# Optimization experiments

Hardware: AMD Instinct MI355X
Metric: run time of the kernel (lower is better)

The kernel has to match this reference:

```python
import jax, jax.numpy as jnp
import numpy as np

N, E, D, H = 100000, 1600000, 128, 2  # nodes, edges, channels (in=out), heads
NEG_SLOPE = 0.2
EPS = 1e-16


def setup_inputs() -> dict:
    key = jax.random.key(0)
    ks = jax.random.split(key, 12)
    s = 1.0 / np.sqrt(D)
    return {
        "x": jax.random.normal(ks[0], (N, D), jnp.float32),
        "edge_index": jax.random.randint(ks[1], (2, E), 0, N, jnp.int64),
        "gamma": jnp.ones((D,), jnp.float32),
        "beta": jnp.zeros((D,), jnp.float32),
        "Wl": jax.random.normal(ks[2], (D, H * D), jnp.float32) * s,
        "bl": jnp.zeros((H * D,), jnp.float32),
        "Wr": jax.random.normal(ks[3], (D, H * D), jnp.float32) * s,
        "br": jnp.zeros((H * D,), jnp.float32),
        "att": jax.random.normal(ks[4], (H, D), jnp.float32) * s,
        "res_W": jax.random.normal(ks[5], (D, D), jnp.float32) * s,
        "bias": jnp.zeros((D,), jnp.float32),
    }


def _segment_softmax(alpha, seg, num_segments):
    m = jax.ops.segment_max(alpha, seg, num_segments=num_segments)
    a = jnp.exp(alpha - m[seg])
    z = jax.ops.segment_sum(a, seg, num_segments=num_segments)
    return a / (z[seg] + EPS)


def reference(x, edge_index, gamma, beta, Wl, bl, Wr, br, att, res_W, bias):
    n = x.shape[0]
    residual = x
    # per-node LayerNorm -> ReLU
    mu = x.mean(-1, keepdims=True)
    var = ((x - mu) ** 2).mean(-1, keepdims=True)
    h = (x - mu) * jax.lax.rsqrt(var + 1e-5) * gamma + beta
    h = jax.nn.relu(h)
    # GATv2: per-node linear transforms [N,H,D]
    xl = (h @ Wl + bl).reshape(n, H, D)  # source-side
    xr = (h @ Wr + br).reshape(n, H, D)  # target-side
    src, dst = edge_index[0], edge_index[1]
    e = jax.nn.leaky_relu(xl[src] + xr[dst], NEG_SLOPE)  # [E,H,D]
    alpha = jnp.einsum('ehd,hd->eh', e, att)             # [E,H]
    alpha = _segment_softmax(alpha, dst, n)
    msg = xl[src] * alpha[..., None]                     # [E,H,D]
    out = jax.ops.segment_sum(msg, dst, num_segments=n)  # [N,H,D]
    out = out.mean(axis=1)                               # concat=False -> mean heads
    out = out + h @ res_W + bias                         # GATv2 internal residual + bias
    return residual + out
```

## Files before the change

### kernel.cpp

```cpp
#include <hip/hip_runtime.h>
#include <hip/hip_bf16.h>
#include <cstdint>
#include <cstddef>

#define DCH 128
#define NHEADS 2
#define NEG_SLOPE 0.2f

typedef __attribute__((ext_vector_type(8))) short short8v;
typedef __attribute__((ext_vector_type(4))) float f32x4;
typedef _Float16 h2 __attribute__((ext_vector_type(2)));
typedef _Float16 h4 __attribute__((ext_vector_type(4)));

__device__ __forceinline__ unsigned short f2bf(float f) {
    union { float f; unsigned int i; } v; v.f = f;
    unsigned int r = v.i + 0x7fffu + ((v.i >> 16) & 1u);
    return (unsigned short)(r >> 16);
}
__device__ __forceinline__ unsigned short f2h_bits(float f) {
    _Float16 h = (_Float16)f;
    union { _Float16 h; unsigned short u; } v; v.h = h; return v.u;
}

__device__ __forceinline__ h2 lrelu2(h2 v, h2 ns) {
    h2 f = v * ns;
#if __has_builtin(__builtin_elementwise_max)
    return __builtin_elementwise_max(v, f);
#else
    h2 r; r[0] = v[0] > f[0] ? v[0] : f[0]; r[1] = v[1] > f[1] ? v[1] : f[1];
    return r;
#endif
}
__device__ __forceinline__ float dot4h(h2 a0, h2 a1, h2 b0, h2 b1) {
#if __has_builtin(__builtin_amdgcn_fdot2)
    return __builtin_amdgcn_fdot2(a0, b0, __builtin_amdgcn_fdot2(a1, b1, 0.f, false), false);
#else
    return (float)a0[0]*(float)b0[0] + (float)a0[1]*(float)b0[1]
         + (float)a1[0]*(float)b1[0] + (float)a1[1]*(float)b1[1];
#endif
}

__device__ __forceinline__ float halfsum(float p) {
    p += __int_as_float(__builtin_amdgcn_update_dpp(
            0, __float_as_int(p), 0x121, 0xF, 0xF, false));
    p += __int_as_float(__builtin_amdgcn_update_dpp(
            0, __float_as_int(p), 0x122, 0xF, 0xF, false));
    p += __int_as_float(__builtin_amdgcn_update_dpp(
            0, __float_as_int(p), 0x124, 0xF, 0xF, false));
    p += __int_as_float(__builtin_amdgcn_update_dpp(
            0, __float_as_int(p), 0x128, 0xF, 0xF, false));
    p += __int_as_float(__builtin_amdgcn_ds_swizzle(
            __float_as_int(p), 0x401F));
    return p;
}

__global__ void prep_and_zero(const float* __restrict__ Wl, const float* __restrict__ Wr,
                              const float* __restrict__ resW,
                              unsigned short* __restrict__ wfrag,
                              int* __restrict__ cnt, int n) {
    if (blockIdx.x >= 40) {
        int i = (blockIdx.x - 40) * 256 + threadIdx.x;
        if (i < n) cnt[i] = 0;
        return;
    }
    int gid  = blockIdx.x * 256 + threadIdx.x;
    int lane = gid & 63;
    int f    = gid >> 6;
    int ks   = f & 3;
    int ct   = f >> 2;
    int col  = ct * 16 + (lane & 15);
    int k0   = ks * 32 + (lane >> 4) * 8;
    const float* W; int ldB, c;
    if (col < 256)      { W = Wl;   ldB = 256; c = col; }
    else if (col < 512) { W = Wr;   ldB = 256; c = col - 256; }
    else                { W = resW; ldB = 128; c = col - 512; }
    unsigned short tmp[8];
#pragma unroll
    for (int j = 0; j < 8; ++j) tmp[j] = f2bf(W[(size_t)(k0 + j) * ldB + c]);
    ushort4* dst = (ushort4*)(wfrag + (size_t)gid * 8);
    dst[0] = make_ushort4(tmp[0], tmp[1], tmp[2], tmp[3]);
    dst[1] = make_ushort4(tmp[4], tmp[5], tmp[6], tmp[7]);
}

__launch_bounds__(256)
__global__ void gemm_fill(const float* __restrict__ x,
                          const float* __restrict__ gamma, const float* __restrict__ beta,
                          const unsigned short* __restrict__ wfrag,
                          const float* __restrict__ bl, const float* __restrict__ br,
                          const float* __restrict__ bias,
                          unsigned short* __restrict__ xl, unsigned short* __restrict__ xr,
                          float* __restrict__ out, int n,
                          const int* __restrict__ srcIdx, const int* __restrict__ dstIdx,
                          int* __restrict__ fillc, int* __restrict__ sbuf, int E, int nrb) {
    __shared__ __align__(16) unsigned short As[128 * 128];

    if ((int)blockIdx.x >= nrb) {
        int i = (blockIdx.x - nrb) * 256 + threadIdx.x;
        int E4 = E >> 2;
        if (i < E4) {
            int4 d = ((const int4*)dstIdx)[i];
            int4 s = ((const int4*)srcIdx)[i];
            sbuf[atomicAdd(&fillc[d.x], 1)] = s.x;
            sbuf[atomicAdd(&fillc[d.y], 1)] = s.y;
            sbuf[atomicAdd(&fillc[d.z], 1)] = s.z;
            sbuf[atomicAdd(&fillc[d.w], 1)] = s.w;
        }
        if (i < (E & 3)) {
            int e = E4 * 4 + i;
            sbuf[atomicAdd(&fillc[dstIdx[e]], 1)] = srcIdx[e];
        }
        return;
    }

    int row0 = blockIdx.x * 128;
    int tid  = threadIdx.x;

    {
        int r  = tid >> 5;
        int k4 = (tid & 31) * 4;
        float4 g4  = *(const float4*)(gamma + k4);
        float4 be4 = *(const float4*)(beta + k4);
#pragma unroll
        for (int i = 0; i < 16; ++i) {
            int row  = r + i * 8;
            int grow = row0 + row;
            float4 a = (grow < n) ? *(const float4*)(x + (size_t)grow * DCH + k4)
                                  : make_float4(0.f, 0.f, 0.f, 0.f);
            float s  = a.x + a.y + a.z + a.w;
            float sq = a.x * a.x + a.y * a.y + a.z * a.z + a.w * a.w;
#pragma unroll
            for (int msk = 16; msk; msk >>= 1) {
                s  += __shfl_xor(s, msk);
                sq += __shfl_xor(sq, msk);
            }
            float mu = s * (1.f / DCH);
            float rs = rsqrtf(sq * (1.f / DCH) - mu * mu + 1e-5f);
            ushort4 u;
            u.x = f2bf(fmaxf((a.x - mu) * rs * g4.x + be4.x, 0.f));
            u.y = f2bf(fmaxf((a.y - mu) * rs * g4.y + be4.y, 0.f));
            u.z = f2bf(fmaxf((a.z - mu) * rs * g4.z + be4.z, 0.f));
            u.w = f2bf(fmaxf((a.w - mu) * rs * g4.w + be4.w, 0.f));
            int byteoff = row * 256 + ((k4 * 2) ^ ((row & 7) << 4));
            *(ushort4*)((char*)As + byteoff) = u;
        }
    }
    __syncthreads();

    int wv = tid >> 6, lane = tid & 63;

    short8v afrag[2][4];
#pragma unroll
    for (int g = 0; g < 2; ++g) {
        int arow = wv * 32 + g * 16 + (lane & 15);
#pragma unroll
        for (int ks = 0; ks < 4; ++ks) {
            int kbyte = (ks * 64 + (lane >> 4) * 16) ^ ((arow & 7) << 4);
            afrag[g][ks] = *(const short8v*)((const char*)As + arow * 256 + kbyte);
        }
    }

    int node0 = row0 + wv * 32 + (lane & 15);
    int node1 = node0 + 16;
    bool v0 = node0 < n, v1 = node1 < n;
    int cq = (lane >> 4) << 2;

#pragma unroll 2
    for (int ct = 0; ct < 40; ++ct) {
        const unsigned short* bp = wfrag + ((size_t)(ct * 4) * 64 + lane) * 8;
        short8v b0 = *(const short8v*)(bp);
        short8v b1 = *(const short8v*)(bp + 64 * 8);
        short8v b2 = *(const short8v*)(bp + 128 * 8);
        short8v b3 = *(const short8v*)(bp + 192 * 8);
        f32x4 acc0 = {0.f, 0.f, 0.f, 0.f};
        f32x4 acc1 = {0.f, 0.f, 0.f, 0.f};
        acc0 = __builtin_amdgcn_mfma_f32_16x16x32_bf16(b0, afrag[0][0], acc0, 0, 0, 0);
        acc1 = __builtin_amdgcn_mfma_f32_16x16x32_bf16(b0, afrag[1][0], acc1, 0, 0, 0);
        acc0 = __builtin_amdgcn_mfma_f32_16x16x32_bf16(b1, afrag[0][1], acc0, 0, 0, 0);
        acc1 = __builtin_amdgcn_mfma_f32_16x16x32_bf16(b1, afrag[1][1], acc1, 0, 0, 0);
        acc0 = __builtin_amdgcn_mfma_f32_16x16x32_bf16(b2, afrag[0][2], acc0, 0, 0, 0);
        acc1 = __builtin_amdgcn_mfma_f32_16x16x32_bf16(b2, afrag[1][2], acc1, 0, 0, 0);
        acc0 = __builtin_amdgcn_mfma_f32_16x16x32_bf16(b3, afrag[0][3], acc0, 0, 0, 0);
        acc1 = __builtin_amdgcn_mfma_f32_16x16x32_bf16(b3, afrag[1][3], acc1, 0, 0, 0);

        int c0 = ct * 16 + cq;
        if (ct < 32) {
            unsigned short* dst; int c; const float* bv;
            if (ct < 16) { dst = xl; c = c0;       bv = bl; }
            else         { dst = xr; c = c0 - 256; bv = br; }
            float4 bb = *(const float4*)(bv + c);
            if (v0) {
                ushort4 u = make_ushort4(f2h_bits(acc0[0] + bb.x), f2h_bits(acc0[1] + bb.y),
                                         f2h_bits(acc0[2] + bb.z), f2h_bits(acc0[3] + bb.w));
                *(ushort4*)(dst + (size_t)node0 * 256 + c) = u;
            }
            if (v1) {
                ushort4 u = make_ushort4(f2h_bits(acc1[0] + bb.x), f2h_bits(acc1[1] + bb.y),
                                         f2h_bits(acc1[2] + bb.z), f2h_bits(acc1[3] + bb.w));
                *(ushort4*)(dst + (size_t)node1 * 256 + c) = u;
            }
        } else {
            int c = c0 - 512;
            float4 bb = *(const float4*)(bias + c);
            if (v0) {
                float4 xv = *(const float4*)(x + (size_t)node0 * DCH + c);
                float4 o = make_float4(acc0[0] + bb.x + xv.x, acc0[1] + bb.y + xv.y,
                                       acc0[2] + bb.z + xv.z, acc0[3] + bb.w + xv.w);
                *(float4*)(out + (size_t)node0 * DCH + c) = o;
            }
            if (v1) {
                float4 xv = *(const float4*)(x + (size_t)node1 * DCH + c);
                float4 o = make_float4(acc1[0] + bb.x + xv.x, acc1[1] + bb.y + xv.y,
                                       acc1[2] + bb.z + xv.z, acc1[3] + bb.w + xv.w);
                *(float4*)(out + (size_t)node1 * DCH + c) = o;
            }
        }
    }
}

__global__ void hist_dst(const int* __restrict__ dst, int* __restrict__ cnt, int E) {
    int i = blockIdx.x * blockDim.x + threadIdx.x;
    int E4 = E >> 2;
    if (i < E4) {
        int4 d = ((const int4*)dst)[i];
        atomicAdd(&cnt[d.x], 1); atomicAdd(&cnt[d.y], 1);
        atomicAdd(&cnt[d.z], 1); atomicAdd(&cnt[d.w], 1);
    }
    if (i < (E & 3)) atomicAdd(&cnt[dst[E4 * 4 + i]], 1);
}

__global__ void scan_block(const int* __restrict__ cnt, int* __restrict__ offs,
                           int* __restrict__ bsum, int n) {
    __shared__ int sm[256];
    int t = threadIdx.x;
    int i = blockIdx.x * 256 + t;
    int v = (i < n) ? cnt[i] : 0;
    sm[t] = v;
    __syncthreads();
#pragma unroll
    for (int d = 1; d < 256; d <<= 1) {
        int add = (t >= d) ? sm[t - d] : 0;
        __syncthreads();
        sm[t] += add;
        __syncthreads();
    }
    if (i < n) offs[i] = sm[t] - v;
    if (t == 255) bsum[blockIdx.x] = sm[t];
}

__global__ void scan_bsum_par(int* __restrict__ bsum, int nb) {
    __shared__ int sm[512];
    int t = threadIdx.x;
    if (nb <= 512) {
        int v = (t < nb) ? bsum[t] : 0;
        sm[t] = v;
        __syncthreads();
#pragma unroll
        for (int d = 1; d < 512; d <<= 1) {
            int add = (t >= d) ? sm[t - d] : 0;
            __syncthreads();
            sm[t] += add;
            __syncthreads();
        }
        if (t < nb) bsum[t] = sm[t] - v;
    } else if (t == 0) {
        int acc = 0;
        for (int i = 0; i < nb; ++i) { int v = bsum[i]; bsum[i] = acc; acc += v; }
    }
}

__global__ void scan_add(int* __restrict__ offs, int* __restrict__ fillc,
                         const int* __restrict__ bsum, int n, int E) {
    int i = blockIdx.x * 256 + threadIdx.x;
    if (i < n) {
        int v = offs[i] + bsum[blockIdx.x];
        offs[i]  = v;
        fillc[i] = v;
    }
    if (i == 0) offs[n] = E;
}

__launch_bounds__(256)
__global__ void gat_aggregate(const int* __restrict__ offs, const int* __restrict__ sbuf,
                              const unsigned short* __restrict__ xl_,
                              const unsigned short* __restrict__ xr_,
                              const float* __restrict__ att,
                              float* __restrict__ out, int n) {
    const _Float16* xl = (const _Float16*)xl_;
    const _Float16* xr = (const _Float16*)xr_;
    int lane = threadIdx.x & 63;
    int wid  = __builtin_amdgcn_readfirstlane((blockIdx.x * blockDim.x + threadIdx.x) >> 6);
    int nw   = (gridDim.x * blockDim.x) >> 6;

    const float LOG2E = 1.4426950408889634f;
    float4 af = *(const float4*)(att + lane * 4);
    h2 av0 = {(_Float16)(af.x * LOG2E), (_Float16)(af.y * LOG2E)};
    h2 av1 = {(_Float16)(af.z * LOG2E), (_Float16)(af.w * LOG2E)};
    h2 ns  = {(_Float16)NEG_SLOPE, (_Float16)NEG_SLOPE};

    for (int t = wid; t < n; t += nw) {
        int beg = offs[t];
        int end = offs[t + 1];
        if (beg == end) continue;
        h4 r4 = *(const h4*)(xr + (size_t)t * 256 + lane * 4);
        h2 r0 = __builtin_shufflevector(r4, r4, 0, 1);
        h2 r1 = __builtin_shufflevector(r4, r4, 2, 3);

        float m = -INFINITY, z = 0.f;
        float4 acc = make_float4(0.f, 0.f, 0.f, 0.f);

        auto process4 = [&](h4 l0, h4 l1, h4 l2, h4 l3) {
            float p0 = dot4h(lrelu2(__builtin_shufflevector(l0, l0, 0, 1) + r0, ns),
                             lrelu2(__builtin_shufflevector(l0, l0, 2, 3) + r1, ns), av0, av1);
            float p1 = dot4h(lrelu2(__builtin_shufflevector(l1, l1, 0, 1) + r0, ns),
                             lrelu2(__builtin_shufflevector(l1, l1, 2, 3) + r1, ns), av0, av1);
            float p2 = dot4h(lrelu2(__builtin_shufflevector(l2, l2, 0, 1) + r0, ns),
                             lrelu2(__builtin_shufflevector(l2, l2, 2, 3) + r1, ns), av0, av1);
            float p3 = dot4h(lrelu2(__builtin_shufflevector(l3, l3, 0, 1) + r0, ns),
                             lrelu2(__builtin_shufflevector(l3, l3, 2, 3) + r1, ns), av0, av1);
            p0 = halfsum(p0); p1 = halfsum(p1); p2 = halfsum(p2); p3 = halfsum(p3);
            float pm = fmaxf(fmaxf(p0, p1), fmaxf(p2, p3));
            if (__any(pm - m > 11.5f)) {
                float mn = fmaxf(m, pm);
                float sc = __builtin_amdgcn_exp2f(m - mn);
                z *= sc;
                acc.x *= sc; acc.y *= sc; acc.z *= sc; acc.w *= sc;
                m = mn;
            }
            float w0 = __builtin_amdgcn_exp2f(p0 - m);
            float w1 = __builtin_amdgcn_exp2f(p1 - m);
            float w2 = __builtin_amdgcn_exp2f(p2 - m);
            float w3 = __builtin_amdgcn_exp2f(p3 - m);
            z += (w0 + w1) + (w2 + w3);
            acc.x = fmaf((float)l0[0], w0, acc.x); acc.y = fmaf((float)l0[1], w0, acc.y);
            acc.z = fmaf((float)l0[2], w0, acc.z); acc.w = fmaf((float)l0[3], w0, acc.w);
            acc.x = fmaf((float)l1[0], w1, acc.x); acc.y = fmaf((float)l1[1], w1, acc.y);
            acc.z = fmaf((float)l1[2], w1, acc.z); acc.w = fmaf((float)l1[3], w1, acc.w);
            acc.x = fmaf((float)l2[0], w2, acc.x); acc.y = fmaf((float)l2[1], w2, acc.y);
            acc.z = fmaf((float)l2[2], w2, acc.z); acc.w = fmaf((float)l2[3], w2, acc.w);
            acc.x = fmaf((float)l3[0], w3, acc.x); acc.y = fmaf((float)l3[1], w3, acc.y);
            acc.z = fmaf((float)l3[2], w3, acc.z); acc.w = fmaf((float)l3[3], w3, acc.w);
        };

        int j = beg;
        h4 c0, c1, c2, c3;
        bool have = (j + 4 <= end);
        if (have) {
            int s0 = sbuf[j], s1 = sbuf[j + 1], s2 = sbuf[j + 2], s3 = sbuf[j + 3];
            c0 = *(const h4*)(xl + (size_t)s0 * 256 + lane * 4);
            c1 = *(const h4*)(xl + (size_t)s1 * 256 + lane * 4);
            c2 = *(const h4*)(xl + (size_t)s2 * 256 + lane * 4);
            c3 = *(const h4*)(xl + (size_t)s3 * 256 + lane * 4);
        }
        for (; j + 8 <= end; j += 4) {
            int s0 = sbuf[j + 4], s1 = sbuf[j + 5], s2 = sbuf[j + 6], s3 = sbuf[j + 7];
            h4 n0 = *(const h4*)(xl + (size_t)s0 * 256 + lane * 4);
            h4 n1 = *(const h4*)(xl + (size_t)s1 * 256 + lane * 4);
            h4 n2 = *(const h4*)(xl + (size_t)s2 * 256 + lane * 4);
            h4 n3 = *(const h4*)(xl + (size_t)s3 * 256 + lane * 4);
            process4(c0, c1, c2, c3);
            c0 = n0; c1 = n1; c2 = n2; c3 = n3;
        }
        if (have) { process4(c0, c1, c2, c3); j += 4; }
        for (; j < end; ++j) {
            int s = sbuf[j];
            h4 l0 = *(const h4*)(xl + (size_t)s * 256 + lane * 4);
            float p = dot4h(lrelu2(__builtin_shufflevector(l0, l0, 0, 1) + r0, ns),
                            lrelu2(__builtin_shufflevector(l0, l0, 2, 3) + r1, ns), av0, av1);
            p = halfsum(p);
            if (__any(p - m > 11.5f)) {
                float mn = fmaxf(m, p);
                float sc = __builtin_amdgcn_exp2f(m - mn);
                z *= sc;
                acc.x *= sc; acc.y *= sc; acc.z *= sc; acc.w *= sc;
                m = mn;
            }
            float w = __builtin_amdgcn_exp2f(p - m);
            z += w;
            acc.x = fmaf((float)l0[0], w, acc.x); acc.y = fmaf((float)l0[1], w, acc.y);
            acc.z = fmaf((float)l0[2], w, acc.z); acc.w = fmaf((float)l0[3], w, acc.w);
        }
        float inv = 0.5f / (z + 1e-16f);
        acc.x *= inv; acc.y *= inv; acc.z *= inv; acc.w *= inv;
        acc.x += __shfl_xor(acc.x, 32);
        acc.y += __shfl_xor(acc.y, 32);
        acc.z += __shfl_xor(acc.z, 32);
        acc.w += __shfl_xor(acc.w, 32);
        if (lane < 32) {
            float4* o = (float4*)(out + (size_t)t * DCH + lane * 4);
            float4 cur = *o;
            cur.x += acc.x; cur.y += acc.y; cur.z += acc.z; cur.w += acc.w;
            *o = cur;
        }
    }
}

extern "C" void kernel_launch(void* const* d_in, const int* in_sizes, int n_in,
                              void* d_out, int out_size, void* d_ws, size_t ws_size,
                              hipStream_t stream) {
    const float* x     = (const float*)d_in[0];
    const int*   ei    = (const int*)d_in[1];
    const float* gamma = (const float*)d_in[2];
    const float* beta  = (const float*)d_in[3];
    const float* Wl    = (const float*)d_in[4];
    const float* bl    = (const float*)d_in[5];
    const float* Wr    = (const float*)d_in[6];
    const float* br    = (const float*)d_in[7];
    const float* att   = (const float*)d_in[8];
    const float* resW  = (const float*)d_in[9];
    const float* bias  = (const float*)d_in[10];
    float* out = (float*)d_out;

    int n = in_sizes[0] / DCH;
    int E = in_sizes[1] / 2;
    const int* src = ei;
    const int* dstIdx = ei + E;

    char* ws = (char*)d_ws;
    size_t off = 0;
    auto alloc = [&](size_t bytes) -> void* {
        void* p = ws + off;
        off = (off + bytes + 255) & ~(size_t)255;
        return p;
    };

    int nb = (n + 255) / 256;

    unsigned short* xl = (unsigned short*)alloc((size_t)n * 256 * 2);
    unsigned short* xr = (unsigned short*)alloc((size_t)n * 256 * 2);
    unsigned short* wfrag = (unsigned short*)alloc(160 * 64 * 8 * 2);
    int* cnt   = (int*)alloc((size_t)n * 4);
    int* offs  = (int*)alloc((size_t)(n + 1) * 4);
    int* bsum  = (int*)alloc((size_t)nb * 4);
    int* fillc = (int*)alloc((size_t)n * 4);
    int* sbuf  = (int*)alloc((size_t)E * 4);

    prep_and_zero<<<40 + nb, 256, 0, stream>>>(Wl, Wr, resW, wfrag, cnt, n);
    int ethr = (E / 4 + 255) / 256 + 1;
    hist_dst<<<ethr, 256, 0, stream>>>(dstIdx, cnt, E);
    scan_block<<<nb, 256, 0, stream>>>(cnt, offs, bsum, n);
    scan_bsum_par<<<1, 512, 0, stream>>>(bsum, nb);
    scan_add<<<nb, 256, 0, stream>>>(offs, fillc, bsum, n, E);

    int nrb = (n + 127) / 128;
    gemm_fill<<<nrb + ethr, 256, 0, stream>>>(x, gamma, beta, wfrag, bl, br, bias,
                                              xl, xr, out, n,
                                              src, dstIdx, fillc, sbuf, E, nrb);
    gat_aggregate<<<2048, 256, 0, stream>>>(offs, sbuf, xl, xr, att, out, n);
}
```

Baseline: 349.9 us.

## Stage GEMM epilogue through swizzled LDS for coalesced 16-byte global stores

The GEMM epilogue now writes the MFMA results (xl/xr in fp16, and the residual output in fp32) into a swizzled shared-memory tile first. The block then copies the tile out row-contiguously with 16-byte vector stores, and adds x to the residual output during that copy. Before, each lane wrote scattered 8- or 16-byte fragments per column tile, which produced poorly coalesced global writes. The cost is extra LDS traffic and several block-wide barriers per column group, which can serialize MFMA work against the stores.

Measured after the change: 324.8 us. 7.2% less time.

```diff
diff --git a/kernel.cpp b/kernel.cpp
--- a/kernel.cpp
+++ b/kernel.cpp
@@ -92,7 +92,7 @@
                           float* __restrict__ out, int n,
                           const int* __restrict__ srcIdx, const int* __restrict__ dstIdx,
                           int* __restrict__ fillc, int* __restrict__ sbuf, int E, int nrb) {
-    __shared__ __align__(16) unsigned short As[128 * 128];
+    __shared__ __align__(16) unsigned char smem[128 * 256];
 
     if ((int)blockIdx.x >= nrb) {
         int i = (blockIdx.x - nrb) * 256 + threadIdx.x;
@@ -114,6 +114,7 @@
 
     int row0 = blockIdx.x * 128;
     int tid  = threadIdx.x;
+    unsigned short* As = (unsigned short*)smem;
 
     {
         int r  = tid >> 5;
@@ -158,62 +159,95 @@
             afrag[g][ks] = *(const short8v*)((const char*)As + arow * 256 + kbyte);
         }
     }
-
-    int node0 = row0 + wv * 32 + (lane & 15);
-    int node1 = node0 + 16;
-    bool v0 = node0 < n, v1 = node1 < n;
+    __syncthreads();
+
+    int nodeL0 = wv * 32 + (lane & 15);
+    int nodeL1 = nodeL0 + 16;
     int cq = (lane >> 4) << 2;
 
-#pragma unroll 2
-    for (int ct = 0; ct < 40; ++ct) {
+    auto mfma_ct = [&](int ct, f32x4& a0, f32x4& a1) {
         const unsigned short* bp = wfrag + ((size_t)(ct * 4) * 64 + lane) * 8;
         short8v b0 = *(const short8v*)(bp);
         short8v b1 = *(const short8v*)(bp + 64 * 8);
         short8v b2 = *(const short8v*)(bp + 128 * 8);
         short8v b3 = *(const short8v*)(bp + 192 * 8);
-        f32x4 acc0 = {0.f, 0.f, 0.f, 0.f};
-        f32x4 acc1 = {0.f, 0.f, 0.f, 0.f};
-        acc0 = __builtin_amdgcn_mfma_f32_16x16x32_bf16(b0, afrag[0][0], acc0, 0, 0, 0);
-        acc1 = __builtin_amdgcn_mfma_f32_16x16x32_bf16(b0, afrag[1][0], acc1, 0, 0, 0);
-        acc0 = __builtin_amdgcn_mfma_f32_16x16x32_bf16(b1, afrag[0][1], acc0, 0, 0, 0);
-        acc1 = __builtin_amdgcn_mfma_f32_16x16x32_bf16(b1, afrag[1][1], acc1, 0, 0, 0);
-        acc0 = __builtin_amdgcn_mfma_f32_16x16x32_bf16(b2, afrag[0][2], acc0, 0, 0, 0);
-        acc1 = __builtin_amdgcn_mfma_f32_16x16x32_bf16(b2, afrag[1][2], acc1, 0, 0, 0);
-        acc0 = __builtin_amdgcn_mfma_f32_16x16x32_bf16(b3, afrag[0][3], acc0, 0, 0, 0);
-        acc1 = __builtin_amdgcn_mfma_f32_16x16x32_bf16(b3, afrag[1][3], acc1, 0, 0, 0);
-
-        int c0 = ct * 16 + cq;
-        if (ct < 32) {
-            unsigned short* dst; int c; const float* bv;
-            if (ct < 16) { dst = xl; c = c0;       bv = bl; }
-            else         { dst = xr; c = c0 - 256; bv = br; }
+        a0 = __builtin_amdgcn_mfma_f32_16x16x32_bf16(b0, afrag[0][0], a0, 0, 0, 0);
+        a1 = __builtin_amdgcn_mfma_f32_16x16x32_bf16(b0, afrag[1][0], a1, 0, 0, 0);
+        a0 = __builtin_amdgcn_mfma_f32_16x16x32_bf16(b1, afrag[0][1], a0, 0, 0, 0);
+        a1 = __builtin_amdgcn_mfma_f32_16x16x32_bf16(b1, afrag[1][1], a1, 0, 0, 0);
+        a0 = __builtin_amdgcn_mfma_f32_16x16x32_bf16(b2, afrag[0][2], a0, 0, 0, 0);
+        a1 = __builtin_amdgcn_mfma_f32_16x16x32_bf16(b2, afrag[1][2], a1, 0, 0, 0);
+        a0 = __builtin_amdgcn_mfma_f32_16x16x32_bf16(b3, afrag[0][3], a0, 0, 0, 0);
+        a1 = __builtin_amdgcn_mfma_f32_16x16x32_bf16(b3, afrag[1][3], a1, 0, 0, 0);
+    };
+
+    for (int fg = 0; fg < 4; ++fg) {
+        unsigned short* dstG = (fg < 2) ? xl : xr;
+        const float* bv      = (fg < 2) ? bl : br;
+        int half = fg & 1;
+#pragma unroll
+        for (int ctl = 0; ctl < 8; ++ctl) {
+            int ct = fg * 8 + ctl;
+            f32x4 acc0 = {0.f, 0.f, 0.f, 0.f};
+            f32x4 acc1 = {0.f, 0.f, 0.f, 0.f};
+            mfma_ct(ct, acc0, acc1);
+            int c = ct * 16 + cq - ((fg < 2) ? 0 : 256);
             float4 bb = *(const float4*)(bv + c);
-            if (v0) {
-                ushort4 u = make_ushort4(f2h_bits(acc0[0] + bb.x), f2h_bits(acc0[1] + bb.y),
-                                         f2h_bits(acc0[2] + bb.z), f2h_bits(acc0[3] + bb.w));
-                *(ushort4*)(dst + (size_t)node0 * 256 + c) = u;
+            int cb = ctl * 32 + cq * 2;
+            ushort4 u0 = make_ushort4(f2h_bits(acc0[0] + bb.x), f2h_bits(acc0[1] + bb.y),
+                                      f2h_bits(acc0[2] + bb.z), f2h_bits(acc0[3] + bb.w));
+            *(ushort4*)(smem + nodeL0 * 256 + (cb ^ ((nodeL0 & 7) << 4))) = u0;
+            ushort4 u1 = make_ushort4(f2h_bits(acc1[0] + bb.x), f2h_bits(acc1[1] + bb.y),
+                                      f2h_bits(acc1[2] + bb.z), f2h_bits(acc1[3] + bb.w));
+            *(ushort4*)(smem + nodeL1 * 256 + (cb ^ ((nodeL1 & 7) << 4))) = u1;
+        }
+        __syncthreads();
+#pragma unroll
+        for (int it = 0; it < 8; ++it) {
+            int chunk = it * 256 + tid;
+            int row  = chunk >> 4;
+            int colb = (chunk & 15) * 16;
+            int grow = row0 + row;
+            if (grow < n) {
+                int4 v = *(const int4*)(smem + row * 256 + (colb ^ ((row & 7) << 4)));
+                *(int4*)((char*)dstG + (size_t)grow * 512 + half * 256 + colb) = v;
             }
-            if (v1) {
-                ushort4 u = make_ushort4(f2h_bits(acc1[0] + bb.x), f2h_bits(acc1[1] + bb.y),
-                                         f2h_bits(acc1[2] + bb.z), f2h_bits(acc1[3] + bb.w));
-                *(ushort4*)(dst + (size_t)node1 * 256 + c) = u;
+        }
+        __syncthreads();
+    }
+
+    for (int fg = 0; fg < 2; ++fg) {
+#pragma unroll
+        for (int ctl = 0; ctl < 4; ++ctl) {
+            int ct = 32 + fg * 4 + ctl;
+            f32x4 acc0 = {0.f, 0.f, 0.f, 0.f};
+            f32x4 acc1 = {0.f, 0.f, 0.f, 0.f};
+            mfma_ct(ct, acc0, acc1);
+            int c = ct * 16 + cq - 512;
+            float4 bb = *(const float4*)(bias + c);
+            int cb = ctl * 64 + cq * 4;
+            float4 w0 = make_float4(acc0[0] + bb.x, acc0[1] + bb.y,
+                                    acc0[2] + bb.z, acc0[3] + bb.w);
+            *(float4*)(smem + nodeL0 * 256 + (cb ^ ((nodeL0 & 7) << 4))) = w0;
+            float4 w1 = make_float4(acc1[0] + bb.x, acc1[1] + bb.y,
+                                    acc1[2] + bb.z, acc1[3] + bb.w);
+            *(float4*)(smem + nodeL1 * 256 + (cb ^ ((nodeL1 & 7) << 4))) = w1;
+        }
+        __syncthreads();
+#pragma unroll
+        for (int it = 0; it < 8; ++it) {
+            int chunk = it * 256 + tid;
+            int row  = chunk >> 4;
+            int colb = (chunk & 15) * 16;
+            int grow = row0 + row;
+            if (grow < n) {
+                float4 v = *(const float4*)(smem + row * 256 + (colb ^ ((row & 7) << 4)));
+                float4 xv = *(const float4*)((const char*)x + (size_t)grow * 512 + fg * 256 + colb);
+                v.x += xv.x; v.y += xv.y; v.z += xv.z; v.w += xv.w;
+                *(float4*)((char*)out + (size_t)grow * 512 + fg * 256 + colb) = v;
             }
-        } else {
-            int c = c0 - 512;
-            float4 bb = *(const float4*)(bias + c);
-            if (v0) {
-                float4 xv = *(const float4*)(x + (size_t)node0 * DCH + c);
-                float4 o = make_float4(acc0[0] + bb.x + xv.x, acc0[1] + bb.y + xv.y,
-                                       acc0[2] + bb.z + xv.z, acc0[3] + bb.w + xv.w);
-                *(float4*)(out + (size_t)node0 * DCH + c) = o;
-            }
-            if (v1) {
-                float4 xv = *(const float4*)(x + (size_t)node1 * DCH + c);
-                float4 o = make_float4(acc1[0] + bb.x + xv.x, acc1[1] + bb.y + xv.y,
-                                       acc1[2] + bb.z + xv.z, acc1[3] + bb.w + xv.w);
-                *(float4*)(out + (size_t)node1 * DCH + c) = o;
-            }
-        }
+        }
+        __syncthreads();
     }
 }
 
```
